# Kernel tuning notes

Measured on AMD Instinct MI355X. Metric: run time of the kernel, lower is better.

Reference implementation:

```python
import jax, jax.numpy as jnp
import numpy as np

B, N, C = 4, 2048, 128
H = 4
HD = C // H
SCALE = HD ** -0.5
NEG = -9e15


def setup_inputs() -> dict:
    key = jax.random.key(0)
    ks = jax.random.split(key, 6)
    x = jax.random.normal(ks[0], (B, N, C), dtype=jnp.float32)
    A = jax.random.randint(ks[1], (N, N), 0, 2, dtype=jnp.int32)
    std = 0.02
    Wq = jax.random.normal(ks[2], (C, C), dtype=jnp.float32) * std
    Wkv = jax.random.normal(ks[3], (2 * C, C), dtype=jnp.float32) * std
    Wp = jax.random.normal(ks[4], (C, C), dtype=jnp.float32) * std
    bp = jnp.zeros((C,), dtype=jnp.float32)
    return {"x": x, "A": A, "Wq": Wq, "Wkv": Wkv, "Wp": Wp, "bp": bp}


def reference(x, A, Wq, Wkv, Wp, bp):
    # q/k/v projections (torch Linear: x @ W.T)
    q = (x @ Wq.T).reshape(B, N, H, HD).transpose(0, 2, 1, 3)      # [B,H,N,HD]
    kv = (x @ Wkv.T).reshape(B, N, 2, H, HD).transpose(2, 0, 3, 1, 4)
    k, v = kv[0], kv[1]                                            # [B,H,N,HD]
    attn = jnp.einsum('bhnd,bhmd->bhnm', q, k) * SCALE             # [B,H,N,N]
    attn = jnp.where(A > 0, attn, NEG)                             # adjacency mask
    attn = jax.nn.softmax(attn, axis=-1)
    out = jnp.einsum('bhnm,bhmd->bhnd', attn, v)                   # [B,H,N,HD]
    out = out.transpose(0, 2, 1, 3).reshape(B, N, C)
    out = out @ Wp.T + bp
    return out + x                                                 # residual
```

## Files before the change

kernel.cpp:

```cpp
#include <hip/hip_runtime.h>
#include <math.h>

constexpr int kB = 4, kN = 2048, kC = 128, kH = 4, kHD = 32;
constexpr float kScaleLog2e = 0.17677669529663687f * 1.4426950408889634f;

typedef __attribute__((ext_vector_type(8))) short bf16x8;
typedef __attribute__((ext_vector_type(4))) float f32x4;

__device__ __forceinline__ float exp2fast(float v) { return __builtin_amdgcn_exp2f(v); }
__device__ __forceinline__ unsigned int cvtpk(float lo, float hi) {
  unsigned int r;
  asm("v_cvt_pk_bf16_f32 %0, %1, %2" : "=v"(r) : "v"(lo), "v"(hi));
  return r;
}
__device__ __forceinline__ float bflo(unsigned int u) {
  union { unsigned int u; float f; } v; v.u = u << 16; return v.f;
}
__device__ __forceinline__ float bfhi(unsigned int u) {
  union { unsigned int u; float f; } v; v.u = u & 0xFFFF0000u; return v.f;
}

__global__ __launch_bounds__(256) void prep_kernel(
    const int* __restrict__ A, const float* __restrict__ Wq,
    const float* __restrict__ Wkv, const float* __restrict__ Wp,
    unsigned long long* __restrict__ Abits, unsigned short* __restrict__ Wallb,
    unsigned short* __restrict__ Wpb) {
  const int bid = blockIdx.x;
  if (bid < 512) {
    const int lane = threadIdx.x & 63;
    const int w0 = bid * 4 + (threadIdx.x >> 6);
    #pragma unroll 4
    for (int k = 0; k < 32; ++k) {
      const int idx = w0 + k * 2048;
      const int row = idx >> 5, c0 = (idx & 31) * 64;
      unsigned long long msk = __ballot(A[(size_t)row * kN + c0 + lane] > 0);
      if (lane == 0) Abits[idx] = msk;
    }
  } else {
    const int i4 = ((bid - 512) * 256 + threadIdx.x) * 4;
    float4 v;
    unsigned short* dst;
    if (i4 < 16384) {
      v = *(const float4*)&Wq[i4];
      v.x *= kScaleLog2e; v.y *= kScaleLog2e; v.z *= kScaleLog2e; v.w *= kScaleLog2e;
      dst = Wallb + i4;
    } else if (i4 < 49152) {
      v = *(const float4*)&Wkv[i4 - 16384];
      dst = Wallb + i4;
    } else {
      v = *(const float4*)&Wp[i4 - 49152];
      dst = Wpb + (i4 - 49152);
    }
    *(uint2*)dst = make_uint2(cvtpk(v.x, v.y), cvtpk(v.z, v.w));
  }
}

__global__ __launch_bounds__(256) void qkv_kernel(
    const float* __restrict__ x, const unsigned short* __restrict__ Wallb,
    unsigned short* __restrict__ qws, unsigned short* __restrict__ kws,
    unsigned short* __restrict__ vtws) {
  __shared__ unsigned short xs[16][136];
  const int t = threadIdx.x;
  const int row0 = blockIdx.x * 16;
  const int b = row0 >> 11;
  {
    const int r = t >> 4, c = (t & 15) * 8;
    const float* src = x + (size_t)(row0 + r) * kC + c;
    float4 a = *(const float4*)src;
    float4 bb = *(const float4*)(src + 4);
    *(uint4*)&xs[r][c] = make_uint4(cvtpk(a.x, a.y), cvtpk(a.z, a.w),
                                    cvtpk(bb.x, bb.y), cvtpk(bb.z, bb.w));
  }
  __syncthreads();
  const int w = t >> 6, l = t & 63, lr = l & 15, g = l >> 4;
  bf16x8 xf[4];
  #pragma unroll
  for (int s = 0; s < 4; ++s) xf[s] = *(const bf16x8*)&xs[lr][s * 32 + g * 8];
  #pragma unroll
  for (int ci = 0; ci < 6; ++ci) {
    const int c0 = (w * 6 + ci) * 16;
    const unsigned short* wr = Wallb + (size_t)(c0 + lr) * kC + g * 8;
    f32x4 acc = {0.f, 0.f, 0.f, 0.f};
    if (c0 < 256) {
      #pragma unroll
      for (int s = 0; s < 4; ++s) {
        bf16x8 wf = *(const bf16x8*)(wr + s * 32);
        acc = __builtin_amdgcn_mfma_f32_16x16x32_bf16(wf, xf[s], acc, 0, 0, 0);
      }
      const int col0 = c0 + g * 4;
      const int h = (col0 & 127) >> 5, hd0 = col0 & 31;
      unsigned short* dst = (col0 < 128) ? qws : kws;
      uint2 pk = make_uint2(cvtpk(acc[0], acc[1]), cvtpk(acc[2], acc[3]));
      *(uint2*)&dst[((size_t)(b * kH + h) * kN + row0 + lr) * kHD + hd0] = pk;
    } else {
      #pragma unroll
      for (int s = 0; s < 4; ++s) {
        bf16x8 wf = *(const bf16x8*)(wr + s * 32);
        acc = __builtin_amdgcn_mfma_f32_16x16x32_bf16(xf[s], wf, acc, 0, 0, 0);
      }
      const int d = (c0 - 256) + lr;
      uint2 pk = make_uint2(cvtpk(acc[0], acc[1]), cvtpk(acc[2], acc[3]));
      *(uint2*)&vtws[((size_t)(b * kH + (d >> 5)) * kHD + (d & 31)) * kN + row0 + g * 4] = pk;
    }
  }
}

__global__ __launch_bounds__(256, 4) void attn_kernel(
    const unsigned short* __restrict__ qws, const unsigned short* __restrict__ kws,
    const unsigned short* __restrict__ vtws,
    const unsigned long long* __restrict__ Abits,
    unsigned short* __restrict__ Opart, float* __restrict__ lws, int tiles) {
  __shared__ unsigned short Psf[4][2][2][64][8];
  const int t = threadIdx.x, w = t >> 6, l = t & 63, lr = l & 15, g = l >> 4;
  const int bh = blockIdx.x, qblk = blockIdx.y, z = blockIdx.z;
  const int q0 = qblk * 128;
  const int qa = q0 + w * 32 + lr, qb = qa + 16;
  const int kt0 = z * tiles;
  const unsigned short* kfp = kws + (size_t)bh * kN * kHD +
                              ((size_t)kt0 * 64 + lr) * kHD + g * 8;
  const unsigned short* vfp0 = vtws + (size_t)bh * kHD * kN + (size_t)lr * kN +
                               kt0 * 64 + g * 8;
  const unsigned short* vfp1 = vfp0 + (size_t)16 * kN;
  bf16x8 qf0 = *(const bf16x8*)&qws[((size_t)bh * kN + qa) * kHD + g * 8];
  bf16x8 qf1 = *(const bf16x8*)&qws[((size_t)bh * kN + qb) * kHD + g * 8];
  const unsigned long long* arow0 = Abits + (size_t)qa * (kN / 64) + kt0;
  const unsigned long long* arow1 = Abits + (size_t)qb * (kN / 64) + kt0;

  f32x4 o0a = {0.f, 0.f, 0.f, 0.f}, o1a = o0a, o2a = o0a;
  f32x4 o0b = o0a, o1b = o0a, o2b = o0a;
  bf16x8 ones;
  #pragma unroll
  for (int i = 0; i < 8; ++i) ones[i] = (short)0x3F80;
  const int gsh = g * 4;
  unsigned short* const psw0 = &Psf[w][0][0][0][0];
  unsigned short* const psw1 = &Psf[w][1][0][0][0];
  const int pbase = (((g >> 1) << 4) | lr) * 8 + (g & 1) * 4;

  #pragma unroll 2
  for (int it = 0; it < tiles; ++it) {
    const unsigned long long mw0 = arow0[it];
    const unsigned long long mw1 = arow1[it];
    const unsigned int wlo0 = ((unsigned int)mw0) >> gsh;
    const unsigned int whi0 = ((unsigned int)(mw0 >> 32)) >> gsh;
    const unsigned int wlo1 = ((unsigned int)mw1) >> gsh;
    const unsigned int whi1 = ((unsigned int)(mw1 >> 32)) >> gsh;
    const unsigned short* ktb = kfp + (size_t)it * 64 * kHD;

    #pragma unroll
    for (int kc = 0; kc < 4; ++kc) {
      bf16x8 kf = *(const bf16x8*)(ktb + (size_t)(kc * 16) * kHD);
      f32x4 z4 = {0.f, 0.f, 0.f, 0.f};
      f32x4 acc0 = __builtin_amdgcn_mfma_f32_16x16x32_bf16(kf, qf0, z4, 0, 0, 0);
      f32x4 acc1 = __builtin_amdgcn_mfma_f32_16x16x32_bf16(kf, qf1, z4, 0, 0, 0);
      const unsigned int word0 = (kc < 2) ? wlo0 : whi0;
      const unsigned int word1 = (kc < 2) ? wlo1 : whi1;
      float p0[4], p1[4];
      #pragma unroll
      for (int i = 0; i < 4; ++i) {
        float e0 = exp2fast(acc0[i]);
        float e1 = exp2fast(acc1[i]);
        int m0, m1;
        asm("v_bfe_i32 %0, %1, %2, 1" : "=v"(m0) : "v"(word0), "n"((kc & 1) * 16 + i));
        asm("v_bfe_i32 %0, %1, %2, 1" : "=v"(m1) : "v"(word1), "n"((kc & 1) * 16 + i));
        union { float f; int u; } u0, u1;
        u0.f = e0; u0.u &= m0; p0[i] = u0.f;
        u1.f = e1; u1.u &= m1; p1[i] = u1.f;
      }
      *(uint2*)(psw0 + kc * 256 + pbase) =
          make_uint2(cvtpk(p0[0], p0[1]), cvtpk(p0[2], p0[3]));
      *(uint2*)(psw1 + kc * 256 + pbase) =
          make_uint2(cvtpk(p1[0], p1[1]), cvtpk(p1[2], p1[3]));
    }
    const unsigned short* vtb0 = vfp0 + it * 64;
    const unsigned short* vtb1 = vfp1 + it * 64;
    #pragma unroll
    for (int ct = 0; ct < 2; ++ct) {
      bf16x8 pf0 = *(const bf16x8*)&Psf[w][0][ct][l][0];
      bf16x8 pf1 = *(const bf16x8*)&Psf[w][1][ct][l][0];
      bf16x8 va = *(const bf16x8*)(vtb0 + ct * 32);
      bf16x8 vb = *(const bf16x8*)(vtb1 + ct * 32);
      o0a = __builtin_amdgcn_mfma_f32_16x16x32_bf16(va, pf0, o0a, 0, 0, 0);
      o1a = __builtin_amdgcn_mfma_f32_16x16x32_bf16(vb, pf0, o1a, 0, 0, 0);
      o2a = __builtin_amdgcn_mfma_f32_16x16x32_bf16(ones, pf0, o2a, 0, 0, 0);
      o0b = __builtin_amdgcn_mfma_f32_16x16x32_bf16(va, pf1, o0b, 0, 0, 0);
      o1b = __builtin_amdgcn_mfma_f32_16x16x32_bf16(vb, pf1, o1b, 0, 0, 0);
      o2b = __builtin_amdgcn_mfma_f32_16x16x32_bf16(ones, pf1, o2b, 0, 0, 0);
    }
  }

  unsigned short* orow0 = Opart + ((size_t)(z * 16 + bh) * kN + qa) * kHD;
  unsigned short* orow1 = Opart + ((size_t)(z * 16 + bh) * kN + qb) * kHD;
  *(uint2*)&orow0[g * 4]      = make_uint2(cvtpk(o0a[0], o0a[1]), cvtpk(o0a[2], o0a[3]));
  *(uint2*)&orow0[16 + g * 4] = make_uint2(cvtpk(o1a[0], o1a[1]), cvtpk(o1a[2], o1a[3]));
  *(uint2*)&orow1[g * 4]      = make_uint2(cvtpk(o0b[0], o0b[1]), cvtpk(o0b[2], o0b[3]));
  *(uint2*)&orow1[16 + g * 4] = make_uint2(cvtpk(o1b[0], o1b[1]), cvtpk(o1b[2], o1b[3]));
  if (g == 0) {
    lws[(size_t)(z * 16 + bh) * kN + qa] = o2a[0];
    lws[(size_t)(z * 16 + bh) * kN + qb] = o2b[0];
  }
}

__global__ __launch_bounds__(256) void proj_kernel(
    const unsigned short* __restrict__ Opart, const float* __restrict__ lws,
    const unsigned short* __restrict__ Wpb, const float* __restrict__ bp,
    const float* __restrict__ x, float* __restrict__ out, int np) {
  const int t = threadIdx.x, w = t >> 6, l = t & 63, lr = l & 15, g = l >> 4;
  const int row0 = blockIdx.x * 16;
  const int b = row0 >> 11;
  bf16x8 af[4];
  #pragma unroll
  for (int s = 0; s < 4; ++s) {
    const int bh = b * kH + s;
    float a0 = 0.f, a1 = 0.f, a2 = 0.f, a3 = 0.f, a4 = 0.f, a5 = 0.f, a6 = 0.f, a7 = 0.f;
    float lacc = 0.f;
    for (int p = 0; p < np; ++p) {
      const size_t base = (size_t)(p * 16 + bh) * kN + row0 + lr;
      const uint4 u = *(const uint4*)&Opart[base * kHD + g * 8];
      lacc += lws[base];
      a0 += bflo(u.x); a1 += bfhi(u.x);
      a2 += bflo(u.y); a3 += bfhi(u.y);
      a4 += bflo(u.z); a5 += bfhi(u.z);
      a6 += bflo(u.w); a7 += bfhi(u.w);
    }
    const float inv = 1.f / fmaxf(lacc, 1e-30f);
    union { uint4 u; bf16x8 v; } cv;
    cv.u = make_uint4(cvtpk(a0 * inv, a1 * inv), cvtpk(a2 * inv, a3 * inv),
                      cvtpk(a4 * inv, a5 * inv), cvtpk(a6 * inv, a7 * inv));
    af[s] = cv.v;
  }
  #pragma unroll
  for (int ci = 0; ci < 2; ++ci) {
    const int c0 = (w * 2 + ci) * 16;
    const unsigned short* wr = Wpb + (size_t)(c0 + lr) * kC + g * 8;
    f32x4 acc = {0.f, 0.f, 0.f, 0.f};
    #pragma unroll
    for (int s = 0; s < 4; ++s) {
      bf16x8 wf = *(const bf16x8*)(wr + s * 32);
      acc = __builtin_amdgcn_mfma_f32_16x16x32_bf16(wf, af[s], acc, 0, 0, 0);
    }
    const int col0 = c0 + g * 4;
    const size_t off = (size_t)(row0 + lr) * kC + col0;
    const float4 xb = *(const float4*)&x[off];
    const float4 bb = *(const float4*)&bp[col0];
    float4 r;
    r.x = acc[0] + bb.x + xb.x;
    r.y = acc[1] + bb.y + xb.y;
    r.z = acc[2] + bb.z + xb.z;
    r.w = acc[3] + bb.w + xb.w;
    *(float4*)&out[off] = r;
  }
}

extern "C" void kernel_launch(void* const* d_in, const int* in_sizes, int n_in,
                              void* d_out, int out_size, void* d_ws, size_t ws_size,
                              hipStream_t stream) {
  const float* x   = (const float*)d_in[0];
  const int*   A   = (const int*)d_in[1];
  const float* Wq  = (const float*)d_in[2];
  const float* Wkv = (const float*)d_in[3];
  const float* Wp  = (const float*)d_in[4];
  const float* bp  = (const float*)d_in[5];
  float* out = (float*)d_out;
  char* ws = (char*)d_ws;

  unsigned short* qws   = (unsigned short*)(ws);
  unsigned short* kws   = (unsigned short*)(ws + (2u << 20));
  unsigned short* vtws  = (unsigned short*)(ws + (4u << 20));
  unsigned long long* Abits = (unsigned long long*)(ws + (6u << 20));
  unsigned short* Wallb = (unsigned short*)(ws + (6u << 20) + (1u << 19));
  unsigned short* Wpb   = Wallb + 384 * 128;
  float*          lws   = (float*)(ws + (7u << 20));
  unsigned short* Opart = (unsigned short*)(ws + (8u << 20));

  const int np = (ws_size >= (16u << 20)) ? 4 : 1;
  const int tiles = 32 / np;

  prep_kernel<<<dim3(576), dim3(256), 0, stream>>>(A, Wq, Wkv, Wp, Abits, Wallb, Wpb);
  qkv_kernel<<<dim3(512), dim3(256), 0, stream>>>(x, Wallb, qws, kws, vtws);
  attn_kernel<<<dim3(16, 16, np), dim3(256), 0, stream>>>(
      qws, kws, vtws, Abits, Opart, lws, tiles);
  proj_kernel<<<dim3(512), dim3(256), 0, stream>>>(Opart, lws, Wpb, bp, x, out, np);
}
```

Before: 67.53 us.

## Stage K/V tiles through double-buffered shared memory with register prefetch

In the attention kernel, each block now loads the next K and V^T tiles once into registers and then into a double-buffered LDS tile. Previously every wave fetched K and V directly from global memory. The adjacency mask words are also prefetched one tile ahead. This is meant to remove redundant per-wave global loads and hide load latency, at the cost of a __syncthreads per tile and extra LDS traffic. The launch-bounds occupancy hint of 4 blocks is also removed.

```diff
diff --git a/kernel.cpp b/kernel.cpp
--- a/kernel.cpp
+++ b/kernel.cpp
@@ -105,26 +105,36 @@
   }
 }
 
-__global__ __launch_bounds__(256, 4) void attn_kernel(
+__global__ __launch_bounds__(256) void attn_kernel(
     const unsigned short* __restrict__ qws, const unsigned short* __restrict__ kws,
     const unsigned short* __restrict__ vtws,
     const unsigned long long* __restrict__ Abits,
     unsigned short* __restrict__ Opart, float* __restrict__ lws, int tiles) {
+  __shared__ unsigned short Ksf[2][4][64][8];
+  __shared__ unsigned short Vtf[2][2][2][64][8];
   __shared__ unsigned short Psf[4][2][2][64][8];
   const int t = threadIdx.x, w = t >> 6, l = t & 63, lr = l & 15, g = l >> 4;
   const int bh = blockIdx.x, qblk = blockIdx.y, z = blockIdx.z;
   const int q0 = qblk * 128;
   const int qa = q0 + w * 32 + lr, qb = qa + 16;
   const int kt0 = z * tiles;
-  const unsigned short* kfp = kws + (size_t)bh * kN * kHD +
-                              ((size_t)kt0 * 64 + lr) * kHD + g * 8;
-  const unsigned short* vfp0 = vtws + (size_t)bh * kHD * kN + (size_t)lr * kN +
-                               kt0 * 64 + g * 8;
-  const unsigned short* vfp1 = vfp0 + (size_t)16 * kN;
+  const unsigned short* kbase = kws + (size_t)bh * kN * kHD;
+  const unsigned short* vbase = vtws + (size_t)bh * kHD * kN;
   bf16x8 qf0 = *(const bf16x8*)&qws[((size_t)bh * kN + qa) * kHD + g * 8];
   bf16x8 qf1 = *(const bf16x8*)&qws[((size_t)bh * kN + qb) * kHD + g * 8];
-  const unsigned long long* arow0 = Abits + (size_t)qa * (kN / 64) + kt0;
-  const unsigned long long* arow1 = Abits + (size_t)qb * (kN / 64) + kt0;
+  const unsigned long long* arow0 = Abits + (size_t)qa * (kN / 64);
+  const unsigned long long* arow1 = Abits + (size_t)qb * (kN / 64);
+
+  const int skc = t >> 6, sl = t & 63;
+  const size_t koff = ((size_t)(skc * 16 + (sl & 15))) * kHD + (sl >> 4) * 8;
+  const int sdh = t >> 7, sct = (t >> 6) & 1;
+  const size_t voff = ((size_t)(sdh * 16 + (sl & 15))) * kN + sct * 32 + (sl >> 4) * 8;
+
+  bf16x8 kreg = *(const bf16x8*)(kbase + (size_t)kt0 * 64 * kHD + koff);
+  bf16x8 vreg = *(const bf16x8*)(vbase + (size_t)kt0 * 64 + voff);
+  *(bf16x8*)&Ksf[0][skc][sl][0] = kreg;
+  *(bf16x8*)&Vtf[0][sdh][sct][sl][0] = vreg;
+  unsigned long long mw0 = arow0[kt0], mw1 = arow1[kt0], mw0n = 0, mw1n = 0;
 
   f32x4 o0a = {0.f, 0.f, 0.f, 0.f}, o1a = o0a, o2a = o0a;
   f32x4 o0b = o0a, o1b = o0a, o2b = o0a;
@@ -138,17 +148,23 @@
 
   #pragma unroll 2
   for (int it = 0; it < tiles; ++it) {
-    const unsigned long long mw0 = arow0[it];
-    const unsigned long long mw1 = arow1[it];
+    const int c = it & 1;
+    const int kt = kt0 + it;
+    __syncthreads();
+    if (it + 1 < tiles) {
+      kreg = *(const bf16x8*)(kbase + (size_t)(kt + 1) * 64 * kHD + koff);
+      vreg = *(const bf16x8*)(vbase + (size_t)(kt + 1) * 64 + voff);
+      mw0n = arow0[kt + 1];
+      mw1n = arow1[kt + 1];
+    }
     const unsigned int wlo0 = ((unsigned int)mw0) >> gsh;
     const unsigned int whi0 = ((unsigned int)(mw0 >> 32)) >> gsh;
     const unsigned int wlo1 = ((unsigned int)mw1) >> gsh;
     const unsigned int whi1 = ((unsigned int)(mw1 >> 32)) >> gsh;
-    const unsigned short* ktb = kfp + (size_t)it * 64 * kHD;
 
     #pragma unroll
     for (int kc = 0; kc < 4; ++kc) {
-      bf16x8 kf = *(const bf16x8*)(ktb + (size_t)(kc * 16) * kHD);
+      bf16x8 kf = *(const bf16x8*)&Ksf[c][kc][l][0];
       f32x4 z4 = {0.f, 0.f, 0.f, 0.f};
       f32x4 acc0 = __builtin_amdgcn_mfma_f32_16x16x32_bf16(kf, qf0, z4, 0, 0, 0);
       f32x4 acc1 = __builtin_amdgcn_mfma_f32_16x16x32_bf16(kf, qf1, z4, 0, 0, 0);
@@ -171,20 +187,24 @@
       *(uint2*)(psw1 + kc * 256 + pbase) =
           make_uint2(cvtpk(p1[0], p1[1]), cvtpk(p1[2], p1[3]));
     }
-    const unsigned short* vtb0 = vfp0 + it * 64;
-    const unsigned short* vtb1 = vfp1 + it * 64;
     #pragma unroll
     for (int ct = 0; ct < 2; ++ct) {
       bf16x8 pf0 = *(const bf16x8*)&Psf[w][0][ct][l][0];
       bf16x8 pf1 = *(const bf16x8*)&Psf[w][1][ct][l][0];
-      bf16x8 va = *(const bf16x8*)(vtb0 + ct * 32);
-      bf16x8 vb = *(const bf16x8*)(vtb1 + ct * 32);
+      bf16x8 va = *(const bf16x8*)&Vtf[c][0][ct][l][0];
+      bf16x8 vb = *(const bf16x8*)&Vtf[c][1][ct][l][0];
       o0a = __builtin_amdgcn_mfma_f32_16x16x32_bf16(va, pf0, o0a, 0, 0, 0);
       o1a = __builtin_amdgcn_mfma_f32_16x16x32_bf16(vb, pf0, o1a, 0, 0, 0);
       o2a = __builtin_amdgcn_mfma_f32_16x16x32_bf16(ones, pf0, o2a, 0, 0, 0);
       o0b = __builtin_amdgcn_mfma_f32_16x16x32_bf16(va, pf1, o0b, 0, 0, 0);
       o1b = __builtin_amdgcn_mfma_f32_16x16x32_bf16(vb, pf1, o1b, 0, 0, 0);
       o2b = __builtin_amdgcn_mfma_f32_16x16x32_bf16(ones, pf1, o2b, 0, 0, 0);
+    }
+    if (it + 1 < tiles) {
+      *(bf16x8*)&Ksf[c ^ 1][skc][sl][0] = kreg;
+      *(bf16x8*)&Vtf[c ^ 1][sdh][sct][sl][0] = vreg;
+      mw0 = mw0n;
+      mw1 = mw1n;
     }
   }
 
```

Result: faster. 58.89 us (-12.8%).
